# Kernel optimization log

Hardware: AMD Instinct MI355X
Metric: run time of the kernel (lower is better)

The kernel has to match this reference:

```python
import jax, jax.numpy as jnp
import numpy as np

NUM_GRAPHS = 3000
L = 7        # num_gc_layers
D = 256      # dims * power
DIMS = 64
POWER = 4
MSG_EPS = 1e-7
LN_EPS = 1e-5


def layer_norm(x, g, b):
    mu = jnp.mean(x, axis=-1, keepdims=True)
    var = jnp.var(x, axis=-1, keepdims=True)
    return (x - mu) * jax.lax.rsqrt(var + LN_EPS) * g + b


def gen_conv(h, src, dst, edge_emb, w, b, n_nodes):
    # GENConv (OGB DeeperGCN), aggr='add', mlp_layers=1:
    #   msg = relu(x_j + e) + eps ; agg = scatter_add ; out = Linear(x + agg)
    msg = jax.nn.relu(h[src] + edge_emb) + MSG_EPS      # [E, D]
    agg = jax.ops.segment_sum(msg, dst, num_segments=n_nodes)
    return (h + agg) @ w + b


def mlp_vn(v, w1, b1, g1, be1, w2, b2, g2, be2):
    # MLP([D, D, D], norm='layer'): Lin -> LN -> ReLU -> Lin -> LN -> ReLU
    v = jax.nn.relu(layer_norm(v @ w1 + b1, g1, be1))
    v = jax.nn.relu(layer_norm(v @ w2 + b2, g2, be2))
    return v


def _forward(x, edge_attr, edge_index, batch, atom_emb, bond_emb, vn_emb,
             gcn_w, gcn_b, norm_g, norm_b, ffn_w, ffn_b,
             vn_w1, vn_b1, vn_g1, vn_be1, vn_w2, vn_b2, vn_g2, vn_be2):
    N = x.shape[0]
    # AtomEncoder / BondEncoder: sum of per-feature embedding gathers
    h = atom_emb[jnp.arange(9), x].sum(axis=1)              # [N, D]
    edge_emb = bond_emb[jnp.arange(3), edge_attr].sum(axis=1)  # [E, D]
    h_init = h

    vn = jnp.broadcast_to(vn_emb[0], (NUM_GRAPHS, D))        # Embedding(1, D) row 0
    h = h + vn[batch]

    src, dst = edge_index[0], edge_index[1]
    out = []
    h = gen_conv(h, src, dst, edge_emb, gcn_w[0], gcn_b[0], N)
    out.append(h @ ffn_w[0] + ffn_b[0])

    for layer in range(1, L):
        h2 = jax.nn.relu(layer_norm(h, norm_g[layer - 1], norm_b[layer - 1]))
        vn_tmp = jax.ops.segment_sum(h2, batch, num_segments=NUM_GRAPHS) + vn
        j = layer - 1
        vn = mlp_vn(vn_tmp, vn_w1[j], vn_b1[j], vn_g1[j], vn_be1[j],
                    vn_w2[j], vn_b2[j], vn_g2[j], vn_be2[j])  # dropout: eval mode -> identity
        h2 = h2 + vn[batch]
        h = gen_conv(h2, src, dst, edge_emb, gcn_w[layer], gcn_b[layer], N) + h
        out.append(h @ ffn_w[layer] + ffn_b[layer])

    h_graph = jnp.concatenate([out[p] for p in range(POWER)], axis=-1)  # [N, 4*64]
    return h_graph, h_init


def setup_inputs() -> dict:
    key = jax.random.key(0)
    ks = jax.random.split(key, 12)
    N, E = 100000, 300000
    s = 0.05
    return dict(
        x=jax.random.randint(ks[0], (N, 9), 0, 64),
        edge_attr=jax.random.randint(ks[1], (E, 3), 0, 8),
        edge_index=jax.random.randint(ks[2], (2, E), 0, N),
        batch=jnp.sort(jax.random.randint(ks[3], (N,), 0, NUM_GRAPHS)),
        atom_emb=jax.random.normal(ks[4], (9, 64, D)) * s,
        bond_emb=jax.random.normal(ks[5], (3, 8, D)) * s,
        vn_emb=jnp.zeros((1, D)),
        gcn_w=jax.random.normal(ks[6], (L, D, D)) * s,
        gcn_b=jnp.zeros((L, D)),
        norm_g=jnp.ones((L, D)),
        norm_b=jnp.zeros((L, D)),
        ffn_w=jax.random.normal(ks[7], (L, D, DIMS)) * s,
        ffn_b=jnp.zeros((L, DIMS)),
        vn_w1=jax.random.normal(ks[8], (L - 1, D, D)) * s,
        vn_b1=jnp.zeros((L - 1, D)),
        vn_g1=jnp.ones((L - 1, D)),
        vn_be1=jnp.zeros((L - 1, D)),
        vn_w2=jax.random.normal(ks[9], (L - 1, D, D)) * s,
        vn_b2=jnp.zeros((L - 1, D)),
        vn_g2=jnp.ones((L - 1, D)),
        vn_be2=jnp.zeros((L - 1, D)),
    )


def reference(x, edge_attr, edge_index, batch, atom_emb, bond_emb, vn_emb,
              gcn_w, gcn_b, norm_g, norm_b, ffn_w, ffn_b,
              vn_w1, vn_b1, vn_g1, vn_be1, vn_w2, vn_b2, vn_g2, vn_be2):
    return _forward(x, edge_attr, edge_index, batch, atom_emb, bond_emb, vn_emb,
                    gcn_w, gcn_b, norm_g, norm_b, ffn_w, ffn_b,
                    vn_w1, vn_b1, vn_g1, vn_be1, vn_w2, vn_b2, vn_g2, vn_be2)
```

## Files before the change

kernel.cpp:

```cpp
#include <hip/hip_runtime.h>
#include <hip/hip_bf16.h>

#define G_NUM 3000

typedef unsigned short u16;
typedef unsigned int u32;

typedef short s16x8 __attribute__((ext_vector_type(8)));
typedef float f32x4 __attribute__((ext_vector_type(4)));

__device__ __forceinline__ float bf2f(u16 u) {
    union { u32 i; float f; } v; v.i = ((u32)u) << 16; return v.f;
}
__device__ __forceinline__ u16 f2bf(float f) {
    union { float f; u32 i; } v; v.f = f;
    u32 r = (v.i + 0x7FFFu + ((v.i >> 16) & 1u)) >> 16;
    return (u16)r;
}
__device__ __forceinline__ float ldf(const void* p, size_t i, int bf) {
    return bf ? bf2f(((const u16*)p)[i]) : ((const float*)p)[i];
}

__device__ __forceinline__ void gl_lds16(const void* g, void* l) {
    __builtin_amdgcn_global_load_lds(
        (const __attribute__((address_space(1))) void*)g,
        (__attribute__((address_space(3))) void*)l, 16, 0, 0);
}

__global__ void k_flag(const u32* __restrict__ norm_g_u32, int* __restrict__ flag) {
    if (threadIdx.x == 0 && blockIdx.x == 0)
        *flag = (norm_g_u32[0] == 0x3F803F80u) ? 1 : 0;
}

__global__ void k_hist(const int* __restrict__ ei, int* __restrict__ cnt, int E) {
    int e = blockIdx.x * blockDim.x + threadIdx.x;
    if (e < E) atomicAdd(&cnt[ei[E + e]], 1);
}

__global__ __launch_bounds__(256) void k_scan_part(const int* __restrict__ cnt,
                                                   int* __restrict__ epos,
                                                   int* __restrict__ part, int N) {
    __shared__ int sh[256];
    int t = threadIdx.x;
    int base = blockIdx.x * 1024 + t * 4;
    int c0 = (base + 0 < N) ? cnt[base + 0] : 0;
    int c1 = (base + 1 < N) ? cnt[base + 1] : 0;
    int c2 = (base + 2 < N) ? cnt[base + 2] : 0;
    int c3 = (base + 3 < N) ? cnt[base + 3] : 0;
    int s4 = c0 + c1 + c2 + c3;
    sh[t] = s4;
    __syncthreads();
    for (int off = 1; off < 256; off <<= 1) {
        int v = (t >= off) ? sh[t - off] : 0;
        __syncthreads();
        sh[t] += v;
        __syncthreads();
    }
    int excl = sh[t] - s4;
    if (base + 0 < N) epos[base + 0] = excl;
    if (base + 1 < N) epos[base + 1] = excl + c0;
    if (base + 2 < N) epos[base + 2] = excl + c0 + c1;
    if (base + 3 < N) epos[base + 3] = excl + c0 + c1 + c2;
    if (t == 255) part[blockIdx.x] = sh[255];
}

__global__ __launch_bounds__(256) void k_scan_top(int* __restrict__ part, int NB) {
    __shared__ int sh[256];
    int t = threadIdx.x;
    int v = (t < NB) ? part[t] : 0;
    sh[t] = v;
    __syncthreads();
    for (int off = 1; off < 256; off <<= 1) {
        int u = (t >= off) ? sh[t - off] : 0;
        __syncthreads();
        sh[t] += u;
        __syncthreads();
    }
    if (t < NB) part[t] = sh[t] - v;
}

__global__ __launch_bounds__(256) void k_scan_fin(int* __restrict__ epos,
                                                  const int* __restrict__ part, int N) {
    int add = part[blockIdx.x];
    int base = blockIdx.x * 1024 + threadIdx.x * 4;
#pragma unroll
    for (int i = 0; i < 4; ++i)
        if (base + i < N) epos[base + i] += add;
}

__global__ void k_scatter(const int* __restrict__ ei, int* __restrict__ epos,
                          int* __restrict__ elist, int E) {
    int e = blockIdx.x * blockDim.x + threadIdx.x;
    if (e < E) {
        int p = atomicAdd(&epos[ei[E + e]], 1);
        elist[p] = e;
    }
}

__global__ void k_atom(const int* __restrict__ x, const void* __restrict__ atom_emb,
                       const void* __restrict__ vn_emb, const int* __restrict__ flagp,
                       float* __restrict__ h, int N) {
    int id = blockIdx.x * blockDim.x + threadIdx.x;
    if (id >= N * 64) return;
    int bf = *flagp;
    int n = id >> 6, d = (id & 63) << 2;
    float s0 = 0.f, s1 = 0.f, s2 = 0.f, s3 = 0.f;
#pragma unroll
    for (int f = 0; f < 9; ++f) {
        size_t row = (size_t)(f * 64 + x[n * 9 + f]) * 256 + d;
        if (bf) {
            ushort4 v = *(const ushort4*)((const u16*)atom_emb + row);
            s0 += bf2f(v.x); s1 += bf2f(v.y); s2 += bf2f(v.z); s3 += bf2f(v.w);
        } else {
            float4 v = *(const float4*)((const float*)atom_emb + row);
            s0 += v.x; s1 += v.y; s2 += v.z; s3 += v.w;
        }
    }
    float4 o = { s0 + ldf(vn_emb, d, bf),     s1 + ldf(vn_emb, d + 1, bf),
                 s2 + ldf(vn_emb, d + 2, bf), s3 + ldf(vn_emb, d + 3, bf) };
    *(float4*)(h + (size_t)n * 256 + d) = o;
}

__global__ void k_hinit(const int* __restrict__ x, const void* __restrict__ atom_emb,
                        const int* __restrict__ flagp, void* __restrict__ d_out_v, int N) {
    int id = blockIdx.x * blockDim.x + threadIdx.x;
    if (id >= N * 64) return;
    int bf = *flagp;
    int n = id >> 6, d = (id & 63) << 2;
    float s0 = 0.f, s1 = 0.f, s2 = 0.f, s3 = 0.f;
#pragma unroll
    for (int f = 0; f < 9; ++f) {
        size_t row = (size_t)(f * 64 + x[n * 9 + f]) * 256 + d;
        if (bf) {
            ushort4 v = *(const ushort4*)((const u16*)atom_emb + row);
            s0 += bf2f(v.x); s1 += bf2f(v.y); s2 += bf2f(v.z); s3 += bf2f(v.w);
        } else {
            float4 v = *(const float4*)((const float*)atom_emb + row);
            s0 += v.x; s1 += v.y; s2 += v.z; s3 += v.w;
        }
    }
    size_t idx = (size_t)N * 256 + (size_t)n * 256 + d;
    if (bf) {
        ushort4 o = { f2bf(s0), f2bf(s1), f2bf(s2), f2bf(s3) };
        *(ushort4*)((u16*)d_out_v + idx) = o;
    } else {
        float4 o = { s0, s1, s2, s3 };
        *(float4*)((float*)d_out_v + idx) = o;
    }
}

__global__ void k_init_vn(const void* __restrict__ vn_emb, const int* __restrict__ flagp,
                          float* __restrict__ vn) {
    int id = blockIdx.x * blockDim.x + threadIdx.x;
    if (id >= G_NUM * 256) return;
    vn[id] = ldf(vn_emb, id & 255, *flagp);
}

__global__ __launch_bounds__(256) void k_agg(
    const int* __restrict__ ei, const int* __restrict__ eattr,
    const int* __restrict__ elist, const int* __restrict__ epos,
    const int* __restrict__ cnt, const void* __restrict__ bond_emb,
    const int* __restrict__ flagp, const float* __restrict__ h,
    const void* __restrict__ d_out_v, u16* __restrict__ xh, u16* __restrict__ xl,
    const float* __restrict__ vnarr, const int* __restrict__ batch,
    int layer0, int E, int N) {
    int bf = *flagp;
    int wv = threadIdx.x >> 6, lane = threadIdx.x & 63;
    int n = blockIdx.x * 4 + wv;
    if (n >= N) return;
    int d = lane << 2;
    size_t ND = (size_t)N * 256;
    float a0 = 0.f, a1 = 0.f, a2 = 0.f, a3 = 0.f;
    int end = epos[n];
    int start = end - cnt[n];
    for (int ee = start; ee < end; ++ee) {
        int e = elist[ee];
        int src = ei[e];
        int b0 = eattr[e * 3], b1 = eattr[e * 3 + 1], b2 = eattr[e * 3 + 2];
        float e0, e1, e2, e3;
        if (bf) {
            const u16* bp = (const u16*)bond_emb;
            ushort4 q0 = *(const ushort4*)(bp + (size_t)b0 * 256 + d);
            ushort4 q1 = *(const ushort4*)(bp + (size_t)(8 + b1) * 256 + d);
            ushort4 q2 = *(const ushort4*)(bp + (size_t)(16 + b2) * 256 + d);
            e0 = bf2f(q0.x) + bf2f(q1.x) + bf2f(q2.x);
            e1 = bf2f(q0.y) + bf2f(q1.y) + bf2f(q2.y);
            e2 = bf2f(q0.z) + bf2f(q1.z) + bf2f(q2.z);
            e3 = bf2f(q0.w) + bf2f(q1.w) + bf2f(q2.w);
        } else {
            const float* bp = (const float*)bond_emb;
            float4 q0 = *(const float4*)(bp + (size_t)b0 * 256 + d);
            float4 q1 = *(const float4*)(bp + (size_t)(8 + b1) * 256 + d);
            float4 q2 = *(const float4*)(bp + (size_t)(16 + b2) * 256 + d);
            e0 = q0.x + q1.x + q2.x; e1 = q0.y + q1.y + q2.y;
            e2 = q0.z + q1.z + q2.z; e3 = q0.w + q1.w + q2.w;
        }
        float h0, h1, h2v, h3;
        if (layer0) {
            float4 hs = *(const float4*)(h + (size_t)src * 256 + d);
            h0 = hs.x; h1 = hs.y; h2v = hs.z; h3 = hs.w;
        } else {
            float4 vv = *(const float4*)(vnarr + (size_t)batch[src] * 256 + d);
            if (bf) {
                ushort4 hs = *(const ushort4*)((const u16*)d_out_v + ND + (size_t)src * 256 + d);
                h0 = bf2f(hs.x) + vv.x; h1 = bf2f(hs.y) + vv.y;
                h2v = bf2f(hs.z) + vv.z; h3 = bf2f(hs.w) + vv.w;
            } else {
                float4 hs = *(const float4*)((const float*)d_out_v + ND + (size_t)src * 256 + d);
                h0 = hs.x + vv.x; h1 = hs.y + vv.y; h2v = hs.z + vv.z; h3 = hs.w + vv.w;
            }
        }
        a0 += fmaxf(h0 + e0, 0.f) + 1e-7f;
        a1 += fmaxf(h1 + e1, 0.f) + 1e-7f;
        a2 += fmaxf(h2v + e2, 0.f) + 1e-7f;
        a3 += fmaxf(h3 + e3, 0.f) + 1e-7f;
    }
    float i0, i1, i2, i3;
    if (layer0) {
        float4 iv = *(const float4*)(h + (size_t)n * 256 + d);
        i0 = iv.x; i1 = iv.y; i2 = iv.z; i3 = iv.w;
    } else {
        float4 vv = *(const float4*)(vnarr + (size_t)batch[n] * 256 + d);
        if (bf) {
            ushort4 iv = *(const ushort4*)((const u16*)d_out_v + ND + (size_t)n * 256 + d);
            i0 = bf2f(iv.x) + vv.x; i1 = bf2f(iv.y) + vv.y;
            i2 = bf2f(iv.z) + vv.z; i3 = bf2f(iv.w) + vv.w;
        } else {
            float4 iv = *(const float4*)((const float*)d_out_v + ND + (size_t)n * 256 + d);
            i0 = iv.x + vv.x; i1 = iv.y + vv.y; i2 = iv.z + vv.z; i3 = iv.w + vv.w;
        }
    }
    float o0 = i0 + a0, o1 = i1 + a1, o2 = i2 + a2, o3 = i3 + a3;
    u16 h0 = f2bf(o0), h1 = f2bf(o1), h2 = f2bf(o2), h3 = f2bf(o3);
    ushort4 hv = { h0, h1, h2, h3 };
    ushort4 lv = { f2bf(o0 - bf2f(h0)), f2bf(o1 - bf2f(h1)),
                   f2bf(o2 - bf2f(h2)), f2bf(o3 - bf2f(h3)) };
    size_t base = (size_t)n * 256 + d;
    *(ushort4*)(xh + base) = hv;
    *(ushort4*)(xl + base) = lv;
}

__global__ void k_prep_w(const void* __restrict__ gcn_w, const void* __restrict__ ffn_w,
                         const int* __restrict__ flagp,
                         u16* __restrict__ cwh, u16* __restrict__ cwl,
                         u16* __restrict__ fwh, u16* __restrict__ fwl) {
    int bf = *flagp;
    int t = blockIdx.x * blockDim.x + threadIdx.x;
    const int CONVT = 4 * 8 * 16 * 64;
    const int FFNT  = 4 * 8 * 4 * 64;
    if (t >= CONVT + FFNT) return;
    bool isc = t < CONVT;
    int u = isc ? t : t - CONVT;
    int lane = u & 63;
    int g = lane >> 4, c16 = lane & 15;
    int ncf = isc ? 16 : 4;
    int fid = u >> 6;
    int cf = fid % ncf;
    int kk = (fid / ncf) & 7;
    int layer = fid / (ncf * 8);
    int ncol = isc ? 256 : 64;
    int col = cf * 16 + c16;
    const void* W = isc ? gcn_w : ffn_w;
    u16* oh = isc ? cwh : fwh;
    u16* ol = isc ? cwl : fwl;
    size_t lbase = (size_t)layer * 256 * ncol;
    size_t o = (size_t)u * 8;
#pragma unroll
    for (int i = 0; i < 8; ++i) {
        int k = kk * 32 + g * 8 + i;
        float v = ldf(W, lbase + (size_t)k * ncol + col, bf);
        u16 hv = f2bf(v);
        oh[o + i] = hv;
        ol[o + i] = f2bf(v - bf2f(hv));
    }
}

__global__ __launch_bounds__(256, 4) void k_mconv(
    const u16* __restrict__ Ah, const u16* __restrict__ Al,
    const u16* __restrict__ cwh, const u16* __restrict__ cwl,
    const u16* __restrict__ fwh, const u16* __restrict__ fwl,
    const void* __restrict__ cbias, const void* __restrict__ fbias,
    const float* __restrict__ res, float* __restrict__ hOut,
    void* __restrict__ d_out_v, const int* __restrict__ flagp,
    const void* __restrict__ ng, const void* __restrict__ nb,
    int cboff, int fboff, int col_off, int goff, int N) {
    __shared__ __align__(16) u16 Shi[32 * 256];
    __shared__ __align__(16) u16 Slo[32 * 256];
    __shared__ float redS[4][2][16];
    __shared__ float redQ[4][2][16];
    int bf = *flagp;
    int t = threadIdx.x;
    int wv = t >> 6, lane = t & 63;
    int g = lane >> 4, c16 = lane & 15;
    int r0 = blockIdx.x * 32;
    size_t ND = (size_t)N * 256;

    {
        int l5 = lane >> 5;
        int cb = (lane & 31) * 16;
#pragma unroll
        for (int j = 0; j < 4; ++j) {
            int rowl = wv * 8 + j * 2 + l5;
            int gr = r0 + rowl; if (gr > N - 1) gr = N - 1;
            int scb = cb ^ ((rowl & 7) << 4);
            const u16* sh = Ah + (size_t)gr * 256 + (scb >> 1);
            const u16* sl = Al + (size_t)gr * 256 + (scb >> 1);
            gl_lds16(sh, &Shi[wv * 2048 + j * 512]);
            gl_lds16(sl, &Slo[wv * 2048 + j * 512]);
        }
    }
    __syncthreads();

    f32x4 acc[2][4] = {};
    if (bf) {
#pragma unroll
        for (int kk = 0; kk < 8; ++kk) {
            s16x8 wh[4];
#pragma unroll
            for (int cf = 0; cf < 4; ++cf)
                wh[cf] = *(const s16x8*)(cwh + ((size_t)((kk * 16 + wv * 4 + cf) * 64 + lane) * 8));
#pragma unroll
            for (int rf = 0; rf < 2; ++rf) {
                int R = rf * 16 + c16;
                int cbyte = (kk * 64 + g * 16) ^ ((R & 7) << 4);
                s16x8 ah = *(const s16x8*)((const char*)Shi + R * 512 + cbyte);
                s16x8 al = *(const s16x8*)((const char*)Slo + R * 512 + cbyte);
#pragma unroll
                for (int cf = 0; cf < 4; ++cf) {
                    acc[rf][cf] = __builtin_amdgcn_mfma_f32_16x16x32_bf16(wh[cf], ah, acc[rf][cf], 0, 0, 0);
                    acc[rf][cf] = __builtin_amdgcn_mfma_f32_16x16x32_bf16(wh[cf], al, acc[rf][cf], 0, 0, 0);
                }
            }
        }
    } else {
#pragma unroll
        for (int kk = 0; kk < 8; ++kk) {
            s16x8 wh[4], wl[4];
#pragma unroll
            for (int cf = 0; cf < 4; ++cf) {
                size_t off = (size_t)((kk * 16 + wv * 4 + cf) * 64 + lane) * 8;
                wh[cf] = *(const s16x8*)(cwh + off);
                wl[cf] = *(const s16x8*)(cwl + off);
            }
#pragma unroll
            for (int rf = 0; rf < 2; ++rf) {
                int R = rf * 16 + c16;
                int cbyte = (kk * 64 + g * 16) ^ ((R & 7) << 4);
                s16x8 ah = *(const s16x8*)((const char*)Shi + R * 512 + cbyte);
                s16x8 al = *(const s16x8*)((const char*)Slo + R * 512 + cbyte);
#pragma unroll
                for (int cf = 0; cf < 4; ++cf) {
                    acc[rf][cf] = __builtin_amdgcn_mfma_f32_16x16x32_bf16(wh[cf], ah, acc[rf][cf], 0, 0, 0);
                    acc[rf][cf] = __builtin_amdgcn_mfma_f32_16x16x32_bf16(wh[cf], al, acc[rf][cf], 0, 0, 0);
                    acc[rf][cf] = __builtin_amdgcn_mfma_f32_16x16x32_bf16(wl[cf], ah, acc[rf][cf], 0, 0, 0);
                    acc[rf][cf] = __builtin_amdgcn_mfma_f32_16x16x32_bf16(wl[cf], al, acc[rf][cf], 0, 0, 0);
                }
            }
        }
    }
    __syncthreads();

    float o[2][4][4];
#pragma unroll
    for (int rf = 0; rf < 2; ++rf) {
        int R = rf * 16 + c16;
        int r = r0 + R;
#pragma unroll
        for (int cf = 0; cf < 4; ++cf) {
            int colb = wv * 64 + cf * 16 + g * 4;
#pragma unroll
            for (int i = 0; i < 4; ++i)
                o[rf][cf][i] = acc[rf][cf][i] + ldf(cbias, cboff + colb + i, bf);
            if (res && r < N) {
                float4 rv = *(const float4*)(res + (size_t)r * 256 + colb);
                o[rf][cf][0] += rv.x; o[rf][cf][1] += rv.y;
                o[rf][cf][2] += rv.z; o[rf][cf][3] += rv.w;
            }
        }
        if (r < N) {
#pragma unroll
            for (int cf = 0; cf < 4; ++cf) {
                int colb = wv * 64 + cf * 16 + g * 4;
                float4 ov = { o[rf][cf][0], o[rf][cf][1], o[rf][cf][2], o[rf][cf][3] };
                *(float4*)(hOut + (size_t)r * 256 + colb) = ov;
            }
        }
    }

    float mu[2], rs_[2];
    if (goff >= 0) {
#pragma unroll
        for (int rf = 0; rf < 2; ++rf) {
            float s = 0.f;
#pragma unroll
            for (int cf = 0; cf < 4; ++cf)
#pragma unroll
                for (int i = 0; i < 4; ++i) s += o[rf][cf][i];
            s += __shfl_xor(s, 16);
            s += __shfl_xor(s, 32);
            if (g == 0) redS[wv][rf][c16] = s;
        }
    }
    __syncthreads();
    if (goff >= 0) {
#pragma unroll
        for (int rf = 0; rf < 2; ++rf) {
            mu[rf] = (redS[0][rf][c16] + redS[1][rf][c16] +
                      redS[2][rf][c16] + redS[3][rf][c16]) * (1.f / 256.f);
            float q = 0.f;
#pragma unroll
            for (int cf = 0; cf < 4; ++cf)
#pragma unroll
                for (int i = 0; i < 4; ++i) {
                    float dv = o[rf][cf][i] - mu[rf];
                    q += dv * dv;
                }
            q += __shfl_xor(q, 16);
            q += __shfl_xor(q, 32);
            if (g == 0) redQ[wv][rf][c16] = q;
        }
    }
    __syncthreads();
    if (goff >= 0) {
#pragma unroll
        for (int rf = 0; rf < 2; ++rf) {
            float var = (redQ[0][rf][c16] + redQ[1][rf][c16] +
                         redQ[2][rf][c16] + redQ[3][rf][c16]) * (1.f / 256.f);
            rs_[rf] = rsqrtf(fmaxf(var, 0.f) + 1e-5f);
            int r = r0 + rf * 16 + c16;
            if (r < N) {
#pragma unroll
                for (int cf = 0; cf < 4; ++cf) {
                    int colb = wv * 64 + cf * 16 + g * 4;
                    float v0 = fmaxf((o[rf][cf][0] - mu[rf]) * rs_[rf] * ldf(ng, goff + colb, bf)     + ldf(nb, goff + colb, bf), 0.f);
                    float v1 = fmaxf((o[rf][cf][1] - mu[rf]) * rs_[rf] * ldf(ng, goff + colb + 1, bf) + ldf(nb, goff + colb + 1, bf), 0.f);
                    float v2 = fmaxf((o[rf][cf][2] - mu[rf]) * rs_[rf] * ldf(ng, goff + colb + 2, bf) + ldf(nb, goff + colb + 2, bf), 0.f);
                    float v3 = fmaxf((o[rf][cf][3] - mu[rf]) * rs_[rf] * ldf(ng, goff + colb + 3, bf) + ldf(nb, goff + colb + 3, bf), 0.f);
                    size_t oi = ND + (size_t)r * 256 + colb;
                    if (bf) {
                        ushort4 q4 = { f2bf(v0), f2bf(v1), f2bf(v2), f2bf(v3) };
                        *(ushort4*)((u16*)d_out_v + oi) = q4;
                    } else {
                        float4 q4 = { v0, v1, v2, v3 };
                        *(float4*)((float*)d_out_v + oi) = q4;
                    }
                }
            }
        }
    }

#pragma unroll
    for (int rf = 0; rf < 2; ++rf) {
        int R = rf * 16 + c16;
#pragma unroll
        for (int cf = 0; cf < 4; ++cf) {
            int colb = wv * 64 + cf * 16 + g * 4;
            float o0 = o[rf][cf][0], o1 = o[rf][cf][1], o2 = o[rf][cf][2], o3 = o[rf][cf][3];
            u16 h0 = f2bf(o0), h1 = f2bf(o1), h2 = f2bf(o2), h3 = f2bf(o3);
            ushort4 hv = { h0, h1, h2, h3 };
            ushort4 lv = { f2bf(o0 - bf2f(h0)), f2bf(o1 - bf2f(h1)),
                           f2bf(o2 - bf2f(h2)), f2bf(o3 - bf2f(h3)) };
            int cbyte = (colb * 2) ^ ((R & 7) << 4);
            *(ushort4*)((char*)Shi + R * 512 + cbyte) = hv;
            *(ushort4*)((char*)Slo + R * 512 + cbyte) = lv;
        }
    }
    __syncthreads();

    f32x4 fa[2] = {};
    if (bf) {
#pragma unroll
        for (int kk = 0; kk < 8; ++kk) {
            s16x8 wh = *(const s16x8*)(fwh + ((size_t)((kk * 4 + wv) * 64 + lane) * 8));
#pragma unroll
            for (int rf = 0; rf < 2; ++rf) {
                int R = rf * 16 + c16;
                int cbyte = (kk * 64 + g * 16) ^ ((R & 7) << 4);
                s16x8 ah = *(const s16x8*)((const char*)Shi + R * 512 + cbyte);
                fa[rf] = __builtin_amdgcn_mfma_f32_16x16x32_bf16(wh, ah, fa[rf], 0, 0, 0);
            }
        }
    } else {
#pragma unroll
        for (int kk = 0; kk < 8; ++kk) {
            size_t off = (size_t)((kk * 4 + wv) * 64 + lane) * 8;
            s16x8 wh = *(const s16x8*)(fwh + off);
            s16x8 wl = *(const s16x8*)(fwl + off);
#pragma unroll
            for (int rf = 0; rf < 2; ++rf) {
                int R = rf * 16 + c16;
                int cbyte = (kk * 64 + g * 16) ^ ((R & 7) << 4);
                s16x8 ah = *(const s16x8*)((const char*)Shi + R * 512 + cbyte);
                s16x8 al = *(const s16x8*)((const char*)Slo + R * 512 + cbyte);
                fa[rf] = __builtin_amdgcn_mfma_f32_16x16x32_bf16(wh, ah, fa[rf], 0, 0, 0);
                fa[rf] = __builtin_amdgcn_mfma_f32_16x16x32_bf16(wh, al, fa[rf], 0, 0, 0);
                fa[rf] = __builtin_amdgcn_mfma_f32_16x16x32_bf16(wl, ah, fa[rf], 0, 0, 0);
                fa[rf] = __builtin_amdgcn_mfma_f32_16x16x32_bf16(wl, al, fa[rf], 0, 0, 0);
            }
        }
    }

    {
        int colb = wv * 16 + g * 4;
        float b0 = ldf(fbias, fboff + colb, bf);
        float b1 = ldf(fbias, fboff + colb + 1, bf);
        float b2 = ldf(fbias, fboff + colb + 2, bf);
        float b3 = ldf(fbias, fboff + colb + 3, bf);
#pragma unroll
        for (int rf = 0; rf < 2; ++rf) {
            int r = r0 + rf * 16 + c16;
            if (r < N) {
                float o0 = fa[rf][0] + b0, o1 = fa[rf][1] + b1;
                float o2 = fa[rf][2] + b2, o3 = fa[rf][3] + b3;
                size_t oi = (size_t)r * 256 + col_off + colb;
                if (bf) {
                    ushort4 q = { f2bf(o0), f2bf(o1), f2bf(o2), f2bf(o3) };
                    *(ushort4*)((u16*)d_out_v + oi) = q;
                } else {
                    float4 q = { o0, o1, o2, o3 };
                    *(float4*)((float*)d_out_v + oi) = q;
                }
            }
        }
    }
}

__global__ __launch_bounds__(256) void k_vn4(
    const void* __restrict__ d_out_v, const int* __restrict__ flagp,
    const int* __restrict__ batch,
    const void* __restrict__ w1, const void* __restrict__ b1,
    const void* __restrict__ g1, const void* __restrict__ be1,
    const void* __restrict__ w2, const void* __restrict__ b2,
    const void* __restrict__ g2, const void* __restrict__ be2,
    float* __restrict__ vn, int woff, int voff, int N) {
    __shared__ float row[4][256];
    __shared__ float red[4][4];
    __shared__ __align__(16) float Ws[32][256];
    int bf = *flagp;
    int t = threadIdx.x;
    int wv = t >> 6, lane = t & 63;
    size_t ND = (size_t)N * 256;

    {
        int gi = blockIdx.x * 4 + wv;
        int lo = 0, hi = N;
        while (lo < hi) { int m = (lo + hi) >> 1; if (batch[m] < gi) lo = m + 1; else hi = m; }
        int s = lo; hi = N;
        while (lo < hi) { int m = (lo + hi) >> 1; if (batch[m] < gi + 1) lo = m + 1; else hi = m; }
        int e = lo;
        int d = lane << 2;
        float4 a = *(const float4*)(vn + (size_t)gi * 256 + d);
        for (int n = s; n < e; ++n) {
            size_t base = ND + (size_t)n * 256 + d;
            if (bf) {
                ushort4 hv = *(const ushort4*)((const u16*)d_out_v + base);
                a.x += bf2f(hv.x); a.y += bf2f(hv.y); a.z += bf2f(hv.z); a.w += bf2f(hv.w);
            } else {
                float4 hv = *(const float4*)((const float*)d_out_v + base);
                a.x += hv.x; a.y += hv.y; a.z += hv.z; a.w += hv.w;
            }
        }
        *(float4*)&row[wv][d] = a;
    }
    __syncthreads();

#pragma unroll 1
    for (int stage = 0; stage < 2; ++stage) {
        const void* W = stage ? w2 : w1;
        const void* B = stage ? b2 : b1;
        const void* G = stage ? g2 : g1;
        const void* BE = stage ? be2 : be1;
        float bb = ldf(B, voff + t, bf);
        float acc[4] = { bb, bb, bb, bb };
#pragma unroll 1
        for (int k0 = 0; k0 < 256; k0 += 32) {
            if (bf) {
                const u32* Wg = (const u32*)((const u16*)W + woff);
#pragma unroll
                for (int i = 0; i < 16; ++i) {
                    int idx = t + i * 256;
                    int k = idx >> 7, c2 = idx & 127;
                    u32 v = Wg[(size_t)(k0 + k) * 128 + c2];
                    Ws[k][2 * c2] = bf2f((u16)(v & 0xffff));
                    Ws[k][2 * c2 + 1] = bf2f((u16)(v >> 16));
                }
            } else {
                const float4* Wg = (const float4*)((const float*)W + woff);
#pragma unroll
                for (int i = 0; i < 8; ++i) {
                    int idx = t + i * 256;
                    int k = idx >> 6, c4 = idx & 63;
                    *(float4*)&Ws[k][4 * c4] = Wg[(size_t)(k0 + k) * 64 + c4];
                }
            }
            __syncthreads();
#pragma unroll
            for (int k = 0; k < 32; ++k) {
                float w = Ws[k][t];
                float r0 = row[0][k0 + k], r1 = row[1][k0 + k];
                float r2 = row[2][k0 + k], r3 = row[3][k0 + k];
                acc[0] = fmaf(r0, w, acc[0]);
                acc[1] = fmaf(r1, w, acc[1]);
                acc[2] = fmaf(r2, w, acc[2]);
                acc[3] = fmaf(r3, w, acc[3]);
            }
            __syncthreads();
        }
        float mu[4], rs_[4];
#pragma unroll
        for (int gr = 0; gr < 4; ++gr) {
            float s = acc[gr];
#pragma unroll
            for (int o = 32; o > 0; o >>= 1) s += __shfl_xor(s, o);
            if (lane == 0) red[wv][gr] = s;
        }
        __syncthreads();
#pragma unroll
        for (int gr = 0; gr < 4; ++gr)
            mu[gr] = (red[0][gr] + red[1][gr] + red[2][gr] + red[3][gr]) * (1.f / 256.f);
        __syncthreads();
#pragma unroll
        for (int gr = 0; gr < 4; ++gr) {
            float dv = acc[gr] - mu[gr];
            float q = dv * dv;
#pragma unroll
            for (int o = 32; o > 0; o >>= 1) q += __shfl_xor(q, o);
            if (lane == 0) red[wv][gr] = q;
        }
        __syncthreads();
        float gn = ldf(G, voff + t, bf), bn = ldf(BE, voff + t, bf);
#pragma unroll
        for (int gr = 0; gr < 4; ++gr) {
            float var = (red[0][gr] + red[1][gr] + red[2][gr] + red[3][gr]) * (1.f / 256.f);
            rs_[gr] = rsqrtf(fmaxf(var, 0.f) + 1e-5f);
        }
        __syncthreads();
#pragma unroll
        for (int gr = 0; gr < 4; ++gr)
            row[gr][t] = fmaxf((acc[gr] - mu[gr]) * rs_[gr] * gn + bn, 0.f);
        __syncthreads();
    }
#pragma unroll
    for (int gr = 0; gr < 4; ++gr)
        vn[(size_t)(blockIdx.x * 4 + gr) * 256 + t] = row[gr][t];
}

extern "C" void kernel_launch(void* const* d_in, const int* in_sizes, int n_in,
                              void* d_out, int out_size, void* d_ws, size_t ws_size,
                              hipStream_t stream) {
    const int* x      = (const int*)d_in[0];
    const int* eattr  = (const int*)d_in[1];
    const int* ei     = (const int*)d_in[2];
    const int* batch  = (const int*)d_in[3];
    const void* atom_emb = d_in[4];
    const void* bond_emb = d_in[5];
    const void* vn_emb   = d_in[6];
    const void* gcn_w    = d_in[7];
    const void* gcn_b    = d_in[8];
    const void* norm_g   = d_in[9];
    const void* norm_b   = d_in[10];
    const void* ffn_w    = d_in[11];
    const void* ffn_b    = d_in[12];
    const void* vn_w1    = d_in[13];
    const void* vn_b1    = d_in[14];
    const void* vn_g1    = d_in[15];
    const void* vn_be1   = d_in[16];
    const void* vn_w2    = d_in[17];
    const void* vn_b2    = d_in[18];
    const void* vn_g2    = d_in[19];
    const void* vn_be2   = d_in[20];

    int N = in_sizes[3];
    int E = in_sizes[2] / 2;
    size_t ND = (size_t)N * 256;
    int NB = (N + 1023) / 1024;

    char* wp = (char*)d_ws;
    int*   flag   = (int*)wp;               wp += 256;
    int*   part   = (int*)wp;               wp += 1024 * 4;
    int*   cnt    = (int*)wp;               wp += (size_t)N * 4;
    int*   epos   = (int*)wp;               wp += (size_t)N * 4;
    int*   elist  = (int*)wp;               wp += (size_t)E * 4;
    float* vn     = (float*)wp;             wp += (size_t)G_NUM * 256 * 4;
    float* vn_tmp = (float*)wp;             wp += (size_t)G_NUM * 256 * 4;
    float* h      = (float*)wp;             wp += ND * 4;
    u16*   xh     = (u16*)wp;
    u16*   xl     = xh + ND;
    (void)vn_tmp;

    size_t wbytes = ((size_t)4 * 65536 * 2 + (size_t)4 * 16384 * 2) * 2;
    size_t wtop   = (ws_size - wbytes) & ~(size_t)255;
    u16* cwh = (u16*)((char*)d_ws + wtop);
    u16* cwl = cwh + (size_t)4 * 65536;
    u16* fwh = cwl + (size_t)4 * 65536;
    u16* fwl = fwh + (size_t)4 * 16384;

    int gE  = (E + 255) / 256;
    int gN4 = (N + 3) / 4;
    int gNv = (N * 64 + 255) / 256;
    int gb  = (N + 31) / 32;

    k_flag<<<1, 64, 0, stream>>>((const u32*)norm_g, flag);
    k_prep_w<<<160, 256, 0, stream>>>(gcn_w, ffn_w, flag, cwh, cwl, fwh, fwl);

    hipMemsetAsync(cnt, 0, (size_t)N * 4, stream);
    k_hist<<<gE, 256, 0, stream>>>(ei, cnt, E);
    k_scan_part<<<NB, 256, 0, stream>>>(cnt, epos, part, N);
    k_scan_top<<<1, 256, 0, stream>>>(part, NB);
    k_scan_fin<<<NB, 256, 0, stream>>>(epos, part, N);
    k_scatter<<<gE, 256, 0, stream>>>(ei, epos, elist, E);

    k_atom<<<gNv, 256, 0, stream>>>(x, atom_emb, vn_emb, flag, h, N);
    k_init_vn<<<(G_NUM * 256 + 255) / 256, 256, 0, stream>>>(vn_emb, flag, vn);

    k_agg<<<gN4, 256, 0, stream>>>(ei, eattr, elist, epos, cnt, bond_emb, flag,
                                   h, d_out, xh, xl, vn, batch, 1, E, N);
    k_mconv<<<gb, 256, 0, stream>>>(xh, xl, cwh, cwl, fwh, fwl, gcn_b, ffn_b,
                                    nullptr, h, d_out, flag, norm_g, norm_b,
                                    0, 0, 0, 0, N);

    for (int l = 1; l < 4; ++l) {
        int j = l - 1;
        k_vn4<<<G_NUM / 4, 256, 0, stream>>>(d_out, flag, batch,
                                             vn_w1, vn_b1, vn_g1, vn_be1,
                                             vn_w2, vn_b2, vn_g2, vn_be2,
                                             vn, j * 65536, j * 256, N);
        k_agg<<<gN4, 256, 0, stream>>>(ei, eattr, elist, epos, cnt, bond_emb, flag,
                                       h, d_out, xh, xl, vn, batch, 0, E, N);
        k_mconv<<<gb, 256, 0, stream>>>(xh, xl, cwh + (size_t)l * 65536,
                                        cwl + (size_t)l * 65536,
                                        fwh + (size_t)l * 16384,
                                        fwl + (size_t)l * 16384,
                                        gcn_b, ffn_b, h, h, d_out, flag,
                                        norm_g, norm_b,
                                        l * 256, l * 64, l * 64,
                                        (l < 3) ? l * 256 : -1, N);
    }
    k_hinit<<<gNv, 256, 0, stream>>>(x, atom_emb, flag, d_out, N);
}
```

Before: 1.755 ms.

## Fuse edge aggregation into matmul kernel and single-pass LayerNorm statistics

Removes the separate k_agg kernel. Each k_mconv block now gathers neighbor messages for its own 32 rows and writes the hi/lo bf16 split directly into shared memory, so the intermediate xh/xl round-trip through global memory and one launch per layer are gone. LayerNorm now computes sum and sum-of-squares in one pass, which drops a barrier. Bias, gamma and beta loads are vectorised, and the residual is prefetched before the matmul. In exchange, the gather runs with less parallelism per block (8 rows serially per wave) and the async global-to-LDS loads are dropped. The one-pass variance is less numerically robust, and h2 buffers are ping-ponged between xh and d_out.

After: 1.940 ms. 1.11x slower.

```diff
diff --git a/kernel.cpp b/kernel.cpp
--- a/kernel.cpp
+++ b/kernel.cpp
@@ -20,11 +20,13 @@
 __device__ __forceinline__ float ldf(const void* p, size_t i, int bf) {
     return bf ? bf2f(((const u16*)p)[i]) : ((const float*)p)[i];
 }
-
-__device__ __forceinline__ void gl_lds16(const void* g, void* l) {
-    __builtin_amdgcn_global_load_lds(
-        (const __attribute__((address_space(1))) void*)g,
-        (__attribute__((address_space(3))) void*)l, 16, 0, 0);
+__device__ __forceinline__ float4 ld4(const void* p, size_t i, int bf) {
+    if (bf) {
+        ushort4 v = *(const ushort4*)((const u16*)p + i);
+        float4 r = { bf2f(v.x), bf2f(v.y), bf2f(v.z), bf2f(v.w) };
+        return r;
+    }
+    return *(const float4*)((const float*)p + i);
 }
 
 __global__ void k_flag(const u32* __restrict__ norm_g_u32, int* __restrict__ flag) {
@@ -99,7 +101,7 @@
 
 __global__ void k_atom(const int* __restrict__ x, const void* __restrict__ atom_emb,
                        const void* __restrict__ vn_emb, const int* __restrict__ flagp,
-                       float* __restrict__ h, int N) {
+                       u16* __restrict__ hAh, u16* __restrict__ hAl, int N) {
     int id = blockIdx.x * blockDim.x + threadIdx.x;
     if (id >= N * 64) return;
     int bf = *flagp;
@@ -116,9 +118,15 @@
             s0 += v.x; s1 += v.y; s2 += v.z; s3 += v.w;
         }
     }
-    float4 o = { s0 + ldf(vn_emb, d, bf),     s1 + ldf(vn_emb, d + 1, bf),
-                 s2 + ldf(vn_emb, d + 2, bf), s3 + ldf(vn_emb, d + 3, bf) };
-    *(float4*)(h + (size_t)n * 256 + d) = o;
+    s0 += ldf(vn_emb, d, bf);     s1 += ldf(vn_emb, d + 1, bf);
+    s2 += ldf(vn_emb, d + 2, bf); s3 += ldf(vn_emb, d + 3, bf);
+    u16 h0 = f2bf(s0), h1 = f2bf(s1), h2 = f2bf(s2), h3 = f2bf(s3);
+    ushort4 hv = { h0, h1, h2, h3 };
+    ushort4 lv = { f2bf(s0 - bf2f(h0)), f2bf(s1 - bf2f(h1)),
+                   f2bf(s2 - bf2f(h2)), f2bf(s3 - bf2f(h3)) };
+    size_t base = (size_t)n * 256 + d;
+    *(ushort4*)(hAh + base) = hv;
+    *(ushort4*)(hAl + base) = lv;
 }
 
 __global__ void k_hinit(const int* __restrict__ x, const void* __restrict__ atom_emb,
@@ -154,90 +162,6 @@
     int id = blockIdx.x * blockDim.x + threadIdx.x;
     if (id >= G_NUM * 256) return;
     vn[id] = ldf(vn_emb, id & 255, *flagp);
-}
-
-__global__ __launch_bounds__(256) void k_agg(
-    const int* __restrict__ ei, const int* __restrict__ eattr,
-    const int* __restrict__ elist, const int* __restrict__ epos,
-    const int* __restrict__ cnt, const void* __restrict__ bond_emb,
-    const int* __restrict__ flagp, const float* __restrict__ h,
-    const void* __restrict__ d_out_v, u16* __restrict__ xh, u16* __restrict__ xl,
-    const float* __restrict__ vnarr, const int* __restrict__ batch,
-    int layer0, int E, int N) {
-    int bf = *flagp;
-    int wv = threadIdx.x >> 6, lane = threadIdx.x & 63;
-    int n = blockIdx.x * 4 + wv;
-    if (n >= N) return;
-    int d = lane << 2;
-    size_t ND = (size_t)N * 256;
-    float a0 = 0.f, a1 = 0.f, a2 = 0.f, a3 = 0.f;
-    int end = epos[n];
-    int start = end - cnt[n];
-    for (int ee = start; ee < end; ++ee) {
-        int e = elist[ee];
-        int src = ei[e];
-        int b0 = eattr[e * 3], b1 = eattr[e * 3 + 1], b2 = eattr[e * 3 + 2];
-        float e0, e1, e2, e3;
-        if (bf) {
-            const u16* bp = (const u16*)bond_emb;
-            ushort4 q0 = *(const ushort4*)(bp + (size_t)b0 * 256 + d);
-            ushort4 q1 = *(const ushort4*)(bp + (size_t)(8 + b1) * 256 + d);
-            ushort4 q2 = *(const ushort4*)(bp + (size_t)(16 + b2) * 256 + d);
-            e0 = bf2f(q0.x) + bf2f(q1.x) + bf2f(q2.x);
-            e1 = bf2f(q0.y) + bf2f(q1.y) + bf2f(q2.y);
-            e2 = bf2f(q0.z) + bf2f(q1.z) + bf2f(q2.z);
-            e3 = bf2f(q0.w) + bf2f(q1.w) + bf2f(q2.w);
-        } else {
-            const float* bp = (const float*)bond_emb;
-            float4 q0 = *(const float4*)(bp + (size_t)b0 * 256 + d);
-            float4 q1 = *(const float4*)(bp + (size_t)(8 + b1) * 256 + d);
-            float4 q2 = *(const float4*)(bp + (size_t)(16 + b2) * 256 + d);
-            e0 = q0.x + q1.x + q2.x; e1 = q0.y + q1.y + q2.y;
-            e2 = q0.z + q1.z + q2.z; e3 = q0.w + q1.w + q2.w;
-        }
-        float h0, h1, h2v, h3;
-        if (layer0) {
-            float4 hs = *(const float4*)(h + (size_t)src * 256 + d);
-            h0 = hs.x; h1 = hs.y; h2v = hs.z; h3 = hs.w;
-        } else {
-            float4 vv = *(const float4*)(vnarr + (size_t)batch[src] * 256 + d);
-            if (bf) {
-                ushort4 hs = *(const ushort4*)((const u16*)d_out_v + ND + (size_t)src * 256 + d);
-                h0 = bf2f(hs.x) + vv.x; h1 = bf2f(hs.y) + vv.y;
-                h2v = bf2f(hs.z) + vv.z; h3 = bf2f(hs.w) + vv.w;
-            } else {
-                float4 hs = *(const float4*)((const float*)d_out_v + ND + (size_t)src * 256 + d);
-                h0 = hs.x + vv.x; h1 = hs.y + vv.y; h2v = hs.z + vv.z; h3 = hs.w + vv.w;
-            }
-        }
-        a0 += fmaxf(h0 + e0, 0.f) + 1e-7f;
-        a1 += fmaxf(h1 + e1, 0.f) + 1e-7f;
-        a2 += fmaxf(h2v + e2, 0.f) + 1e-7f;
-        a3 += fmaxf(h3 + e3, 0.f) + 1e-7f;
-    }
-    float i0, i1, i2, i3;
-    if (layer0) {
-        float4 iv = *(const float4*)(h + (size_t)n * 256 + d);
-        i0 = iv.x; i1 = iv.y; i2 = iv.z; i3 = iv.w;
-    } else {
-        float4 vv = *(const float4*)(vnarr + (size_t)batch[n] * 256 + d);
-        if (bf) {
-            ushort4 iv = *(const ushort4*)((const u16*)d_out_v + ND + (size_t)n * 256 + d);
-            i0 = bf2f(iv.x) + vv.x; i1 = bf2f(iv.y) + vv.y;
-            i2 = bf2f(iv.z) + vv.z; i3 = bf2f(iv.w) + vv.w;
-        } else {
-            float4 iv = *(const float4*)((const float*)d_out_v + ND + (size_t)n * 256 + d);
-            i0 = iv.x + vv.x; i1 = iv.y + vv.y; i2 = iv.z + vv.z; i3 = iv.w + vv.w;
-        }
-    }
-    float o0 = i0 + a0, o1 = i1 + a1, o2 = i2 + a2, o3 = i3 + a3;
-    u16 h0 = f2bf(o0), h1 = f2bf(o1), h2 = f2bf(o2), h3 = f2bf(o3);
-    ushort4 hv = { h0, h1, h2, h3 };
-    ushort4 lv = { f2bf(o0 - bf2f(h0)), f2bf(o1 - bf2f(h1)),
-                   f2bf(o2 - bf2f(h2)), f2bf(o3 - bf2f(h3)) };
-    size_t base = (size_t)n * 256 + d;
-    *(ushort4*)(xh + base) = hv;
-    *(ushort4*)(xl + base) = lv;
 }
 
 __global__ void k_prep_w(const void* __restrict__ gcn_w, const void* __restrict__ ffn_w,
@@ -276,14 +200,20 @@
 }
 
 __global__ __launch_bounds__(256, 4) void k_mconv(
-    const u16* __restrict__ Ah, const u16* __restrict__ Al,
+    const int* __restrict__ ei, const int* __restrict__ eattr,
+    const int* __restrict__ elist, const int* __restrict__ epos,
+    const int* __restrict__ cnt, const void* __restrict__ bond_emb,
+    const int* __restrict__ batch, const float* __restrict__ vnarr,
+    const u16* __restrict__ hAh, const u16* __restrict__ hAl,
+    u16* __restrict__ xbuf,
     const u16* __restrict__ cwh, const u16* __restrict__ cwl,
     const u16* __restrict__ fwh, const u16* __restrict__ fwl,
     const void* __restrict__ cbias, const void* __restrict__ fbias,
     const float* __restrict__ res, float* __restrict__ hOut,
     void* __restrict__ d_out_v, const int* __restrict__ flagp,
     const void* __restrict__ ng, const void* __restrict__ nb,
-    int cboff, int fboff, int col_off, int goff, int N) {
+    int cboff, int fboff, int col_off, int goff,
+    int rsel, int wsel, int layer0, int N) {
     __shared__ __align__(16) u16 Shi[32 * 256];
     __shared__ __align__(16) u16 Slo[32 * 256];
     __shared__ float redS[4][2][16];
@@ -296,17 +226,99 @@
     size_t ND = (size_t)N * 256;
 
     {
-        int l5 = lane >> 5;
-        int cb = (lane & 31) * 16;
-#pragma unroll
-        for (int j = 0; j < 4; ++j) {
-            int rowl = wv * 8 + j * 2 + l5;
-            int gr = r0 + rowl; if (gr > N - 1) gr = N - 1;
-            int scb = cb ^ ((rowl & 7) << 4);
-            const u16* sh = Ah + (size_t)gr * 256 + (scb >> 1);
-            const u16* sl = Al + (size_t)gr * 256 + (scb >> 1);
-            gl_lds16(sh, &Shi[wv * 2048 + j * 512]);
-            gl_lds16(sl, &Slo[wv * 2048 + j * 512]);
+        const u16* h2rb = rsel ? (const u16*)d_out_v + ND : (const u16*)xbuf;
+        const float* h2rf = rsel ? (const float*)d_out_v + ND : (const float*)xbuf;
+        int d = lane << 2;
+#pragma unroll 1
+        for (int j = 0; j < 8; ++j) {
+            int R = wv * 8 + j;
+            int n = r0 + R;
+            float o0 = 0.f, o1 = 0.f, o2 = 0.f, o3 = 0.f;
+            if (n < N) {
+                int end = epos[n];
+                int start = end - cnt[n];
+                float a0 = 0.f, a1 = 0.f, a2 = 0.f, a3 = 0.f;
+                for (int ee = start; ee < end; ++ee) {
+                    int e = elist[ee];
+                    int src = ei[e];
+                    int b0 = eattr[e * 3], b1 = eattr[e * 3 + 1], b2 = eattr[e * 3 + 2];
+                    float e0, e1, e2, e3;
+                    if (bf) {
+                        const u16* bp = (const u16*)bond_emb;
+                        ushort4 q0 = *(const ushort4*)(bp + (size_t)b0 * 256 + d);
+                        ushort4 q1 = *(const ushort4*)(bp + (size_t)(8 + b1) * 256 + d);
+                        ushort4 q2 = *(const ushort4*)(bp + (size_t)(16 + b2) * 256 + d);
+                        e0 = bf2f(q0.x) + bf2f(q1.x) + bf2f(q2.x);
+                        e1 = bf2f(q0.y) + bf2f(q1.y) + bf2f(q2.y);
+                        e2 = bf2f(q0.z) + bf2f(q1.z) + bf2f(q2.z);
+                        e3 = bf2f(q0.w) + bf2f(q1.w) + bf2f(q2.w);
+                    } else {
+                        const float* bp = (const float*)bond_emb;
+                        float4 q0 = *(const float4*)(bp + (size_t)b0 * 256 + d);
+                        float4 q1 = *(const float4*)(bp + (size_t)(8 + b1) * 256 + d);
+                        float4 q2 = *(const float4*)(bp + (size_t)(16 + b2) * 256 + d);
+                        e0 = q0.x + q1.x + q2.x; e1 = q0.y + q1.y + q2.y;
+                        e2 = q0.z + q1.z + q2.z; e3 = q0.w + q1.w + q2.w;
+                    }
+                    float h0, h1, h2v, h3;
+                    if (layer0) {
+                        ushort4 hh = *(const ushort4*)(hAh + (size_t)src * 256 + d);
+                        ushort4 hl = *(const ushort4*)(hAl + (size_t)src * 256 + d);
+                        h0 = bf2f(hh.x) + bf2f(hl.x); h1 = bf2f(hh.y) + bf2f(hl.y);
+                        h2v = bf2f(hh.z) + bf2f(hl.z); h3 = bf2f(hh.w) + bf2f(hl.w);
+                    } else {
+                        float4 vv = *(const float4*)(vnarr + (size_t)batch[src] * 256 + d);
+                        if (bf) {
+                            ushort4 hs = *(const ushort4*)(h2rb + (size_t)src * 256 + d);
+                            h0 = bf2f(hs.x) + vv.x; h1 = bf2f(hs.y) + vv.y;
+                            h2v = bf2f(hs.z) + vv.z; h3 = bf2f(hs.w) + vv.w;
+                        } else {
+                            float4 hs = *(const float4*)(h2rf + (size_t)src * 256 + d);
+                            h0 = hs.x + vv.x; h1 = hs.y + vv.y;
+                            h2v = hs.z + vv.z; h3 = hs.w + vv.w;
+                        }
+                    }
+                    a0 += fmaxf(h0 + e0, 0.f) + 1e-7f;
+                    a1 += fmaxf(h1 + e1, 0.f) + 1e-7f;
+                    a2 += fmaxf(h2v + e2, 0.f) + 1e-7f;
+                    a3 += fmaxf(h3 + e3, 0.f) + 1e-7f;
+                }
+                if (layer0) {
+                    ushort4 hh = *(const ushort4*)(hAh + (size_t)n * 256 + d);
+                    ushort4 hl = *(const ushort4*)(hAl + (size_t)n * 256 + d);
+                    o0 = bf2f(hh.x) + bf2f(hl.x) + a0; o1 = bf2f(hh.y) + bf2f(hl.y) + a1;
+                    o2 = bf2f(hh.z) + bf2f(hl.z) + a2; o3 = bf2f(hh.w) + bf2f(hl.w) + a3;
+                } else {
+                    float4 vv = *(const float4*)(vnarr + (size_t)batch[n] * 256 + d);
+                    if (bf) {
+                        ushort4 iv = *(const ushort4*)(h2rb + (size_t)n * 256 + d);
+                        o0 = bf2f(iv.x) + vv.x + a0; o1 = bf2f(iv.y) + vv.y + a1;
+                        o2 = bf2f(iv.z) + vv.z + a2; o3 = bf2f(iv.w) + vv.w + a3;
+                    } else {
+                        float4 iv = *(const float4*)(h2rf + (size_t)n * 256 + d);
+                        o0 = iv.x + vv.x + a0; o1 = iv.y + vv.y + a1;
+                        o2 = iv.z + vv.z + a2; o3 = iv.w + vv.w + a3;
+                    }
+                }
+            }
+            u16 q0 = f2bf(o0), q1 = f2bf(o1), q2 = f2bf(o2), q3 = f2bf(o3);
+            ushort4 hv = { q0, q1, q2, q3 };
+            ushort4 lv = { f2bf(o0 - bf2f(q0)), f2bf(o1 - bf2f(q1)),
+                           f2bf(o2 - bf2f(q2)), f2bf(o3 - bf2f(q3)) };
+            int cb = (d * 2) ^ ((R & 7) << 4);
+            *(ushort4*)((char*)Shi + R * 512 + cb) = hv;
+            *(ushort4*)((char*)Slo + R * 512 + cb) = lv;
+        }
+    }
+
+    float4 rv[2][4];
+    if (res) {
+#pragma unroll
+        for (int rf = 0; rf < 2; ++rf) {
+            int r = r0 + rf * 16 + c16; if (r > N - 1) r = N - 1;
+#pragma unroll
+            for (int cf = 0; cf < 4; ++cf)
+                rv[rf][cf] = *(const float4*)(res + (size_t)r * 256 + wv * 64 + cf * 16 + g * 4);
         }
     }
     __syncthreads();
@@ -361,20 +373,23 @@
     __syncthreads();
 
     float o[2][4][4];
+    float4 bvv[4];
+#pragma unroll
+    for (int cf = 0; cf < 4; ++cf)
+        bvv[cf] = ld4(cbias, cboff + wv * 64 + cf * 16 + g * 4, bf);
 #pragma unroll
     for (int rf = 0; rf < 2; ++rf) {
         int R = rf * 16 + c16;
         int r = r0 + R;
 #pragma unroll
         for (int cf = 0; cf < 4; ++cf) {
-            int colb = wv * 64 + cf * 16 + g * 4;
-#pragma unroll
-            for (int i = 0; i < 4; ++i)
-                o[rf][cf][i] = acc[rf][cf][i] + ldf(cbias, cboff + colb + i, bf);
+            o[rf][cf][0] = acc[rf][cf][0] + bvv[cf].x;
+            o[rf][cf][1] = acc[rf][cf][1] + bvv[cf].y;
+            o[rf][cf][2] = acc[rf][cf][2] + bvv[cf].z;
+            o[rf][cf][3] = acc[rf][cf][3] + bvv[cf].w;
             if (res && r < N) {
-                float4 rv = *(const float4*)(res + (size_t)r * 256 + colb);
-                o[rf][cf][0] += rv.x; o[rf][cf][1] += rv.y;
-                o[rf][cf][2] += rv.z; o[rf][cf][3] += rv.w;
+                o[rf][cf][0] += rv[rf][cf].x; o[rf][cf][1] += rv[rf][cf].y;
+                o[rf][cf][2] += rv[rf][cf].z; o[rf][cf][3] += rv[rf][cf].w;
             }
         }
         if (r < N) {
@@ -387,62 +402,58 @@
         }
     }
 
-    float mu[2], rs_[2];
     if (goff >= 0) {
 #pragma unroll
         for (int rf = 0; rf < 2; ++rf) {
-            float s = 0.f;
+            float s = 0.f, q = 0.f;
 #pragma unroll
             for (int cf = 0; cf < 4; ++cf)
 #pragma unroll
-                for (int i = 0; i < 4; ++i) s += o[rf][cf][i];
-            s += __shfl_xor(s, 16);
-            s += __shfl_xor(s, 32);
-            if (g == 0) redS[wv][rf][c16] = s;
+                for (int i = 0; i < 4; ++i) {
+                    float v = o[rf][cf][i];
+                    s += v; q += v * v;
+                }
+            s += __shfl_xor(s, 16); s += __shfl_xor(s, 32);
+            q += __shfl_xor(q, 16); q += __shfl_xor(q, 32);
+            if (g == 0) { redS[wv][rf][c16] = s; redQ[wv][rf][c16] = q; }
         }
     }
     __syncthreads();
     if (goff >= 0) {
+        u16* h2wb = wsel ? (u16*)d_out_v + ND : xbuf;
+        float* h2wf = wsel ? (float*)d_out_v + ND : (float*)xbuf;
+        float4 gg[4], bb[4];
+#pragma unroll
+        for (int cf = 0; cf < 4; ++cf) {
+            int colb = wv * 64 + cf * 16 + g * 4;
+            gg[cf] = ld4(ng, goff + colb, bf);
+            bb[cf] = ld4(nb, goff + colb, bf);
+        }
 #pragma unroll
         for (int rf = 0; rf < 2; ++rf) {
-            mu[rf] = (redS[0][rf][c16] + redS[1][rf][c16] +
-                      redS[2][rf][c16] + redS[3][rf][c16]) * (1.f / 256.f);
-            float q = 0.f;
-#pragma unroll
-            for (int cf = 0; cf < 4; ++cf)
-#pragma unroll
-                for (int i = 0; i < 4; ++i) {
-                    float dv = o[rf][cf][i] - mu[rf];
-                    q += dv * dv;
-                }
-            q += __shfl_xor(q, 16);
-            q += __shfl_xor(q, 32);
-            if (g == 0) redQ[wv][rf][c16] = q;
-        }
-    }
-    __syncthreads();
-    if (goff >= 0) {
-#pragma unroll
-        for (int rf = 0; rf < 2; ++rf) {
-            float var = (redQ[0][rf][c16] + redQ[1][rf][c16] +
-                         redQ[2][rf][c16] + redQ[3][rf][c16]) * (1.f / 256.f);
-            rs_[rf] = rsqrtf(fmaxf(var, 0.f) + 1e-5f);
+            float s4 = (redS[0][rf][c16] + redS[1][rf][c16] +
+                        redS[2][rf][c16] + redS[3][rf][c16]);
+            float q4 = (redQ[0][rf][c16] + redQ[1][rf][c16] +
+                        redQ[2][rf][c16] + redQ[3][rf][c16]);
+            float mu = s4 * (1.f / 256.f);
+            float var = q4 * (1.f / 256.f) - mu * mu;
+            float rs = rsqrtf(fmaxf(var, 0.f) + 1e-5f);
             int r = r0 + rf * 16 + c16;
             if (r < N) {
 #pragma unroll
                 for (int cf = 0; cf < 4; ++cf) {
                     int colb = wv * 64 + cf * 16 + g * 4;
-                    float v0 = fmaxf((o[rf][cf][0] - mu[rf]) * rs_[rf] * ldf(ng, goff + colb, bf)     + ldf(nb, goff + colb, bf), 0.f);
-                    float v1 = fmaxf((o[rf][cf][1] - mu[rf]) * rs_[rf] * ldf(ng, goff + colb + 1, bf) + ldf(nb, goff + colb + 1, bf), 0.f);
-                    float v2 = fmaxf((o[rf][cf][2] - mu[rf]) * rs_[rf] * ldf(ng, goff + colb + 2, bf) + ldf(nb, goff + colb + 2, bf), 0.f);
-                    float v3 = fmaxf((o[rf][cf][3] - mu[rf]) * rs_[rf] * ldf(ng, goff + colb + 3, bf) + ldf(nb, goff + colb + 3, bf), 0.f);
-                    size_t oi = ND + (size_t)r * 256 + colb;
+                    float v0 = fmaxf((o[rf][cf][0] - mu) * rs * gg[cf].x + bb[cf].x, 0.f);
+                    float v1 = fmaxf((o[rf][cf][1] - mu) * rs * gg[cf].y + bb[cf].y, 0.f);
+                    float v2 = fmaxf((o[rf][cf][2] - mu) * rs * gg[cf].z + bb[cf].z, 0.f);
+                    float v3 = fmaxf((o[rf][cf][3] - mu) * rs * gg[cf].w + bb[cf].w, 0.f);
+                    size_t oi = (size_t)r * 256 + colb;
                     if (bf) {
-                        ushort4 q4 = { f2bf(v0), f2bf(v1), f2bf(v2), f2bf(v3) };
-                        *(ushort4*)((u16*)d_out_v + oi) = q4;
+                        ushort4 q4v = { f2bf(v0), f2bf(v1), f2bf(v2), f2bf(v3) };
+                        *(ushort4*)(h2wb + oi) = q4v;
                     } else {
-                        float4 q4 = { v0, v1, v2, v3 };
-                        *(float4*)((float*)d_out_v + oi) = q4;
+                        float4 q4v = { v0, v1, v2, v3 };
+                        *(float4*)(h2wf + oi) = q4v;
                     }
                 }
             }
@@ -502,16 +513,13 @@
 
     {
         int colb = wv * 16 + g * 4;
-        float b0 = ldf(fbias, fboff + colb, bf);
-        float b1 = ldf(fbias, fboff + colb + 1, bf);
-        float b2 = ldf(fbias, fboff + colb + 2, bf);
-        float b3 = ldf(fbias, fboff + colb + 3, bf);
+        float4 fb = ld4(fbias, fboff + colb, bf);
 #pragma unroll
         for (int rf = 0; rf < 2; ++rf) {
             int r = r0 + rf * 16 + c16;
             if (r < N) {
-                float o0 = fa[rf][0] + b0, o1 = fa[rf][1] + b1;
-                float o2 = fa[rf][2] + b2, o3 = fa[rf][3] + b3;
+                float o0 = fa[rf][0] + fb.x, o1 = fa[rf][1] + fb.y;
+                float o2 = fa[rf][2] + fb.z, o3 = fa[rf][3] + fb.w;
                 size_t oi = (size_t)r * 256 + col_off + colb;
                 if (bf) {
                     ushort4 q = { f2bf(o0), f2bf(o1), f2bf(o2), f2bf(o3) };
@@ -526,8 +534,8 @@
 }
 
 __global__ __launch_bounds__(256) void k_vn4(
-    const void* __restrict__ d_out_v, const int* __restrict__ flagp,
-    const int* __restrict__ batch,
+    const void* __restrict__ d_out_v, const u16* __restrict__ xbuf, int rsel,
+    const int* __restrict__ flagp, const int* __restrict__ batch,
     const void* __restrict__ w1, const void* __restrict__ b1,
     const void* __restrict__ g1, const void* __restrict__ be1,
     const void* __restrict__ w2, const void* __restrict__ b2,
@@ -542,6 +550,8 @@
     size_t ND = (size_t)N * 256;
 
     {
+        const u16* h2b = rsel ? (const u16*)d_out_v + ND : xbuf;
+        const float* h2f = rsel ? (const float*)d_out_v + ND : (const float*)xbuf;
         int gi = blockIdx.x * 4 + wv;
         int lo = 0, hi = N;
         while (lo < hi) { int m = (lo + hi) >> 1; if (batch[m] < gi) lo = m + 1; else hi = m; }
@@ -551,12 +561,12 @@
         int d = lane << 2;
         float4 a = *(const float4*)(vn + (size_t)gi * 256 + d);
         for (int n = s; n < e; ++n) {
-            size_t base = ND + (size_t)n * 256 + d;
+            size_t base = (size_t)n * 256 + d;
             if (bf) {
-                ushort4 hv = *(const ushort4*)((const u16*)d_out_v + base);
+                ushort4 hv = *(const ushort4*)(h2b + base);
                 a.x += bf2f(hv.x); a.y += bf2f(hv.y); a.z += bf2f(hv.z); a.w += bf2f(hv.w);
             } else {
-                float4 hv = *(const float4*)((const float*)d_out_v + base);
+                float4 hv = *(const float4*)(h2f + base);
                 a.x += hv.x; a.y += hv.y; a.z += hv.z; a.w += hv.w;
             }
         }
@@ -696,7 +706,6 @@
     u16* fwl = fwh + (size_t)4 * 16384;
 
     int gE  = (E + 255) / 256;
-    int gN4 = (N + 3) / 4;
     int gNv = (N * 64 + 255) / 256;
     int gb  = (N + 31) / 32;
 
@@ -710,31 +719,30 @@
     k_scan_fin<<<NB, 256, 0, stream>>>(epos, part, N);
     k_scatter<<<gE, 256, 0, stream>>>(ei, epos, elist, E);
 
-    k_atom<<<gNv, 256, 0, stream>>>(x, atom_emb, vn_emb, flag, h, N);
+    k_atom<<<gNv, 256, 0, stream>>>(x, atom_emb, vn_emb, flag, xh, xl, N);
     k_init_vn<<<(G_NUM * 256 + 255) / 256, 256, 0, stream>>>(vn_emb, flag, vn);
 
-    k_agg<<<gN4, 256, 0, stream>>>(ei, eattr, elist, epos, cnt, bond_emb, flag,
-                                   h, d_out, xh, xl, vn, batch, 1, E, N);
-    k_mconv<<<gb, 256, 0, stream>>>(xh, xl, cwh, cwl, fwh, fwl, gcn_b, ffn_b,
+    k_mconv<<<gb, 256, 0, stream>>>(ei, eattr, elist, epos, cnt, bond_emb, batch, vn,
+                                    xh, xl, xh, cwh, cwl, fwh, fwl, gcn_b, ffn_b,
                                     nullptr, h, d_out, flag, norm_g, norm_b,
-                                    0, 0, 0, 0, N);
+                                    0, 0, 0, 0 , 1 , 1 ,
+                                    1 , N);
 
     for (int l = 1; l < 4; ++l) {
         int j = l - 1;
-        k_vn4<<<G_NUM / 4, 256, 0, stream>>>(d_out, flag, batch,
+        int rsel = (l == 2) ? 0 : 1;
+        int wsel = (l == 1) ? 0 : 1;
+        k_vn4<<<G_NUM / 4, 256, 0, stream>>>(d_out, xh, rsel, flag, batch,
                                              vn_w1, vn_b1, vn_g1, vn_be1,
                                              vn_w2, vn_b2, vn_g2, vn_be2,
                                              vn, j * 65536, j * 256, N);
-        k_agg<<<gN4, 256, 0, stream>>>(ei, eattr, elist, epos, cnt, bond_emb, flag,
-                                       h, d_out, xh, xl, vn, batch, 0, E, N);
-        k_mconv<<<gb, 256, 0, stream>>>(xh, xl, cwh + (size_t)l * 65536,
-                                        cwl + (size_t)l * 65536,
-                                        fwh + (size_t)l * 16384,
-                                        fwl + (size_t)l * 16384,
-                                        gcn_b, ffn_b, h, h, d_out, flag,
-                                        norm_g, norm_b,
+        k_mconv<<<gb, 256, 0, stream>>>(ei, eattr, elist, epos, cnt, bond_emb, batch, vn,
+                                        xh, xl, xh,
+                                        cwh + (size_t)l * 65536, cwl + (size_t)l * 65536,
+                                        fwh + (size_t)l * 16384, fwl + (size_t)l * 16384,
+                                        gcn_b, ffn_b, h, h, d_out, flag, norm_g, norm_b,
                                         l * 256, l * 64, l * 64,
-                                        (l < 3) ? l * 256 : -1, N);
+                                        (l < 3) ? l * 256 : -1, rsel, wsel, 0, N);
     }
     k_hinit<<<gNv, 256, 0, stream>>>(x, atom_emb, flag, d_out, N);
 }
```
